# Kernel tuning notes

Hardware: AMD Instinct MI355X
Metric: run time of the kernel (lower is better)

The kernel has to match this reference:

```python
import jax, jax.numpy as jnp
import numpy as np

NEG_SLOPE = 0.01  # nn.LeakyReLU() default; module's alpha=-0.2 is unused
MASK_VAL = -1e12

N, IN_DIM, OUT_DIM = 4096, 512, 64


def setup_inputs() -> dict:
    key = jax.random.key(0)
    k1, k2, k3, k4 = jax.random.split(key, 4)
    input_h = jax.random.normal(k1, (N, IN_DIM), dtype=jnp.float32)
    adj = jax.random.randint(k2, (N, N), 0, 2, dtype=jnp.int32)
    W = jax.random.normal(k3, (IN_DIM, OUT_DIM), dtype=jnp.float32) * 0.05
    a = jax.random.normal(k4, (2 * OUT_DIM, 1), dtype=jnp.float32) * 0.05
    return {"input_h": input_h, "adj": adj, "W": W, "a": a}


def reference(input_h, adj, W, a):
    h = input_h @ W  # [N, D]
    D = h.shape[1]
    # e_ij = leakyrelu(a^T [h_i || h_j]) = leakyrelu(a1.h_i + a2.h_j)
    a1, a2 = a[:D, 0], a[D:, 0]
    s1 = h @ a1  # [N]
    s2 = h @ a2  # [N]
    e = s1[:, None] + s2[None, :]  # [N, N]
    e = jnp.where(e >= 0, e, NEG_SLOPE * e)  # LeakyReLU(0.01)
    scores = jnp.where(adj > 0, e, MASK_VAL)
    attention = jax.nn.softmax(scores, axis=1)
    # dropout omitted (eval mode / deterministic reference)
    return attention @ h  # [N, D]
```

## Files before the change

### kernel.cpp

```cpp
#include <hip/hip_runtime.h>
#include <hip/hip_bf16.h>

#define NN 4096
#define IN_DIM 512
#define OUT_D 64
#define LOG2E 1.44269504088896340736f

typedef __attribute__((ext_vector_type(8))) short short8v;
typedef __attribute__((ext_vector_type(4))) float f32x4;

__device__ __forceinline__ short to_bf16_rne(float x) {
  unsigned u = __builtin_bit_cast(unsigned, x);
  u = (u + 0x7FFFu + ((u >> 16) & 1u)) >> 16;
  return (short)u;
}
__device__ __forceinline__ float bf16_to_f(short h) {
  unsigned u = ((unsigned)(unsigned short)h) << 16;
  return __builtin_bit_cast(float, u);
}
__device__ __forceinline__ unsigned fkey(float f) {
  unsigned u = __builtin_bit_cast(unsigned, f);
  return u ^ ((unsigned)((int)u >> 31) | 0x80000000u);
}
__device__ __forceinline__ float funkey(unsigned k) {
  unsigned u = (k >> 31) ? (k ^ 0x80000000u) : ~k;
  return __builtin_bit_cast(float, u);
}

__global__ __launch_bounds__(256) void k_wpack(
    const float* __restrict__ W, short* __restrict__ Ahi, short* __restrict__ Alo,
    unsigned* __restrict__ s2key)
{
  int tid = blockIdx.x * 256 + threadIdx.x;
  if (tid == 0) *s2key = 0u;
  int l = tid & 63, t = (tid >> 6) & 15, m = tid >> 10;
  int dd = m * 16 + (l & 15);
  int kbase = t * 32 + 8 * (l >> 4);
  short8v hi, lo;
  #pragma unroll
  for (int r = 0; r < 8; ++r) {
    float w = W[(size_t)(kbase + r) * OUT_D + dd];
    short h = to_bf16_rne(w);
    hi[r] = h;
    lo[r] = to_bf16_rne(w - bf16_to_f(h));
  }
  *(short8v*)(Ahi + (size_t)tid * 8) = hi;
  *(short8v*)(Alo + (size_t)tid * 8) = lo;
}

__global__ __launch_bounds__(256) void k_h_mfma(
    const float* __restrict__ X,
    const short* __restrict__ Ahi, const short* __restrict__ Alo,
    const float* __restrict__ a,
    short* __restrict__ hbT, float* __restrict__ s1, float* __restrict__ s2,
    unsigned* __restrict__ s2key)
{
  __shared__ short xhi[16 * 512];
  __shared__ short xlo[16 * 512];
  __shared__ float sm1[4][16], sm2[4][16];
  int tid = threadIdx.x;
  int m = tid >> 6, l = tid & 63, lo = l & 15, g = l >> 4;
  int row0 = blockIdx.x * 16;

  #pragma unroll
  for (int i = 0; i < 4; ++i) {
    int flat = i * 2048 + tid * 8;
    int r = flat >> 9, k = flat & 511;
    float f[8];
    *(float4*)(f)     = *(const float4*)(X + (size_t)row0 * IN_DIM + flat);
    *(float4*)(f + 4) = *(const float4*)(X + (size_t)row0 * IN_DIM + flat + 4);
    short8v hi, lov;
    #pragma unroll
    for (int q = 0; q < 8; ++q) {
      short h = to_bf16_rne(f[q]);
      hi[q] = h;
      lov[q] = to_bf16_rne(f[q] - bf16_to_f(h));
    }
    int chunk = k >> 3;
    int dst = (r << 9) + ((chunk ^ (r & 7)) << 3);
    *(short8v*)(xhi + dst) = hi;
    *(short8v*)(xlo + dst) = lov;
  }
  __syncthreads();

  f32x4 acc = {0.f, 0.f, 0.f, 0.f};
  const short* ah = Ahi + ((size_t)(m * 16) * 64 + l) * 8;
  const short* al = Alo + ((size_t)(m * 16) * 64 + l) * 8;
  #pragma unroll
  for (int t = 0; t < 16; ++t) {
    int c = t * 4 + g;
    int src = (lo << 9) + ((c ^ (lo & 7)) << 3);
    short8v bhi = *(const short8v*)(xhi + src);
    short8v blo = *(const short8v*)(xlo + src);
    short8v fhi = *(const short8v*)(ah + (size_t)t * 64 * 8);
    short8v flo = *(const short8v*)(al + (size_t)t * 64 * 8);
    acc = __builtin_amdgcn_mfma_f32_16x16x32_bf16(fhi, bhi, acc, 0, 0, 0);
    acc = __builtin_amdgcn_mfma_f32_16x16x32_bf16(fhi, blo, acc, 0, 0, 0);
    acc = __builtin_amdgcn_mfma_f32_16x16x32_bf16(flo, bhi, acc, 0, 0, 0);
  }

  float p1 = 0.f, p2 = 0.f;
  #pragma unroll
  for (int q = 0; q < 4; ++q) {
    int d = m * 16 + 4 * g + q;
    hbT[(size_t)d * NN + row0 + lo] = to_bf16_rne(acc[q]);
    p1 = fmaf(acc[q], a[d], p1);
    p2 = fmaf(acc[q], a[OUT_D + d], p2);
  }
  p1 += __shfl_xor(p1, 16); p1 += __shfl_xor(p1, 32);
  p2 += __shfl_xor(p2, 16); p2 += __shfl_xor(p2, 32);
  if (l < 16) { sm1[m][l] = p1; sm2[m][l] = p2; }
  __syncthreads();
  if (tid < 16) {
    float v1 = (sm1[0][tid] + sm1[1][tid] + sm1[2][tid] + sm1[3][tid]) * LOG2E;
    float v2 = (sm2[0][tid] + sm2[1][tid] + sm2[2][tid] + sm2[3][tid]) * LOG2E;
    s1[row0 + tid] = v1;
    s2[row0 + tid] = v2;
    float v = v2;
    #pragma unroll
    for (int off = 8; off >= 1; off >>= 1) v = fmaxf(v, __shfl_xor(v, off));
    if (tid == 0) atomicMax(s2key, fkey(v));
  }
}

template<int JCHUNK>
__global__ __launch_bounds__(256) void k_attn(
    const int* __restrict__ adj, const short* __restrict__ hbT,
    const float* __restrict__ s1, const float* __restrict__ s2,
    const unsigned* __restrict__ s2keyp,
    float* __restrict__ accp, float* __restrict__ lpart)
{
  constexpr int NIT = JCHUNK / 32;
  int w  = threadIdx.x >> 6;
  int l  = threadIdx.x & 63;
  int lo = l & 15, g = l >> 4;
  int part  = blockIdx.y;
  int ibase = blockIdx.x * 64 + w * 16;
  int row   = ibase + lo;

  float s1v = s1[row];
  float x = s1v + funkey(*s2keyp);
  float M = fmaxf(x, 0.01f * x);

  f32x4 c0 = {0.f,0.f,0.f,0.f}, c1 = {0.f,0.f,0.f,0.f};
  f32x4 c2 = {0.f,0.f,0.f,0.f}, c3 = {0.f,0.f,0.f,0.f};
  float lsum = 0.f;

  const int* adjrow = adj + (size_t)row * NN;
  int jj = part * JCHUNK + g * 8;

  int4 pa0[2], pa1[2]; float4 ps0[2], ps1[2];
  #pragma unroll
  for (int p = 0; p < 2; ++p) {
    int j = jj + p * 32;
    pa0[p] = *(const int4*)(adjrow + j);
    pa1[p] = *(const int4*)(adjrow + j + 4);
    ps0[p] = *(const float4*)(s2 + j);
    ps1[p] = *(const float4*)(s2 + j + 4);
  }

  #pragma unroll
  for (int it = 0; it < NIT; ++it) {
    const int buf = it & 1;
    int4 a0 = pa0[buf], a1 = pa1[buf];
    float4 t0 = ps0[buf], t1 = ps1[buf];
    if (it + 2 < NIT) {
      int j = jj + (it + 2) * 32;
      pa0[buf] = *(const int4*)(adjrow + j);
      pa1[buf] = *(const int4*)(adjrow + j + 4);
      ps0[buf] = *(const float4*)(s2 + j);
      ps1[buf] = *(const float4*)(s2 + j + 4);
    }
    int jc = jj + it * 32;

    short8v b0 = *(const short8v*)(hbT + ((size_t)(lo)      << 12) + jc);
    short8v b1 = *(const short8v*)(hbT + ((size_t)(16 + lo) << 12) + jc);
    short8v b2 = *(const short8v*)(hbT + ((size_t)(32 + lo) << 12) + jc);
    short8v b3 = *(const short8v*)(hbT + ((size_t)(48 + lo) << 12) + jc);

    int av[8]; float sv[8];
    *(int4*)(av) = a0;  *(int4*)(av + 4) = a1;
    *(float4*)(sv) = t0; *(float4*)(sv + 4) = t1;

    short8v af;
    #pragma unroll
    for (int r = 0; r < 8; ++r) {
      float y = s1v + sv[r];
      float e = fmaxf(y, 0.01f * y);
      float p = exp2f(e - M);
      p = (av[r] > 0) ? p : 0.f;
      lsum += p;
      af[r] = to_bf16_rne(p);
    }

    c0 = __builtin_amdgcn_mfma_f32_16x16x32_bf16(af, b0, c0, 0, 0, 0);
    c1 = __builtin_amdgcn_mfma_f32_16x16x32_bf16(af, b1, c1, 0, 0, 0);
    c2 = __builtin_amdgcn_mfma_f32_16x16x32_bf16(af, b2, c2, 0, 0, 0);
    c3 = __builtin_amdgcn_mfma_f32_16x16x32_bf16(af, b3, c3, 0, 0, 0);
  }

  lsum += __shfl_xor(lsum, 16);
  lsum += __shfl_xor(lsum, 32);
  if (l < 16) lpart[(size_t)part * NN + ibase + l] = lsum;

  float* ap = accp + ((size_t)part * NN + ibase) * OUT_D;
  #pragma unroll
  for (int q = 0; q < 4; ++q) {
    int ri = g * 4 + q;
    ap[ri * OUT_D +  0 + lo] = c0[q];
    ap[ri * OUT_D + 16 + lo] = c1[q];
    ap[ri * OUT_D + 32 + lo] = c2[q];
    ap[ri * OUT_D + 48 + lo] = c3[q];
  }
}

__global__ __launch_bounds__(256) void k_attn_rt(
    const int* __restrict__ adj, const short* __restrict__ hbT,
    const float* __restrict__ s1, const float* __restrict__ s2,
    const unsigned* __restrict__ s2keyp,
    float* __restrict__ accp, float* __restrict__ lpart, int jchunk)
{
  int w  = threadIdx.x >> 6;
  int l  = threadIdx.x & 63;
  int lo = l & 15, g = l >> 4;
  int part  = blockIdx.y;
  int ibase = blockIdx.x * 64 + w * 16;
  int row   = ibase + lo;
  float s1v = s1[row];
  float x = s1v + funkey(*s2keyp);
  float M = fmaxf(x, 0.01f * x);
  f32x4 c0 = {0.f,0.f,0.f,0.f}, c1 = {0.f,0.f,0.f,0.f};
  f32x4 c2 = {0.f,0.f,0.f,0.f}, c3 = {0.f,0.f,0.f,0.f};
  float lsum = 0.f;
  const int* adjrow = adj + (size_t)row * NN;
  int jj = part * jchunk + g * 8;
  for (int js = 0; js < jchunk; js += 32, jj += 32) {
    int4 a0 = *(const int4*)(adjrow + jj);
    int4 a1 = *(const int4*)(adjrow + jj + 4);
    float4 t0 = *(const float4*)(s2 + jj);
    float4 t1 = *(const float4*)(s2 + jj + 4);
    short8v b0 = *(const short8v*)(hbT + ((size_t)(lo)      << 12) + jj);
    short8v b1 = *(const short8v*)(hbT + ((size_t)(16 + lo) << 12) + jj);
    short8v b2 = *(const short8v*)(hbT + ((size_t)(32 + lo) << 12) + jj);
    short8v b3 = *(const short8v*)(hbT + ((size_t)(48 + lo) << 12) + jj);
    int av[8]; float sv[8];
    *(int4*)(av) = a0;  *(int4*)(av + 4) = a1;
    *(float4*)(sv) = t0; *(float4*)(sv + 4) = t1;
    short8v af;
    #pragma unroll
    for (int r = 0; r < 8; ++r) {
      float y = s1v + sv[r];
      float e = fmaxf(y, 0.01f * y);
      float p = exp2f(e - M);
      p = (av[r] > 0) ? p : 0.f;
      lsum += p;
      af[r] = to_bf16_rne(p);
    }
    c0 = __builtin_amdgcn_mfma_f32_16x16x32_bf16(af, b0, c0, 0, 0, 0);
    c1 = __builtin_amdgcn_mfma_f32_16x16x32_bf16(af, b1, c1, 0, 0, 0);
    c2 = __builtin_amdgcn_mfma_f32_16x16x32_bf16(af, b2, c2, 0, 0, 0);
    c3 = __builtin_amdgcn_mfma_f32_16x16x32_bf16(af, b3, c3, 0, 0, 0);
  }
  lsum += __shfl_xor(lsum, 16);
  lsum += __shfl_xor(lsum, 32);
  if (l < 16) lpart[(size_t)part * NN + ibase + l] = lsum;
  float* ap = accp + ((size_t)part * NN + ibase) * OUT_D;
  #pragma unroll
  for (int q = 0; q < 4; ++q) {
    int ri = g * 4 + q;
    ap[ri * OUT_D +  0 + lo] = c0[q];
    ap[ri * OUT_D + 16 + lo] = c1[q];
    ap[ri * OUT_D + 32 + lo] = c2[q];
    ap[ri * OUT_D + 48 + lo] = c3[q];
  }
}

__global__ __launch_bounds__(256) void k_combine(
    const float* __restrict__ accp, const float* __restrict__ lpart,
    float* __restrict__ out, int npart)
{
  int idx = blockIdx.x * 256 + threadIdx.x;
  int i = idx >> 6;
  float s = 0.f, li = 0.f;
  for (int p = 0; p < npart; ++p) {
    s  += accp[(size_t)p * (NN * OUT_D) + idx];
    li += lpart[(size_t)p * NN + i];
  }
  out[idx] = s / li;
}

extern "C" void kernel_launch(void* const* d_in, const int* in_sizes, int n_in,
                              void* d_out, int out_size, void* d_ws, size_t ws_size,
                              hipStream_t stream)
{
  const float* X   = (const float*)d_in[0];
  const int*   adj = (const int*)d_in[1];
  const float* W   = (const float*)d_in[2];
  const float* a   = (const float*)d_in[3];
  float* out = (float*)d_out;

  char* ws = (char*)d_ws;
  size_t off = 0;
  float* s1  = (float*)(ws + off); off += NN * 4;
  float* s2  = (float*)(ws + off); off += NN * 4;
  unsigned* s2key = (unsigned*)(ws + off); off += 64;
  short* hbT = (short*)(ws + off); off += (size_t)OUT_D * NN * 2;
  short* Ahi = (short*)(ws + off); off += 4096 * 8 * 2;
  short* Alo = (short*)(ws + off); off += 4096 * 8 * 2;
  size_t fixed = off;

  size_t per_part = (size_t)(NN * OUT_D + NN) * 4;
  int npart = 1;
  for (int p = 16; p >= 1; p >>= 1)
    if (fixed + (size_t)p * per_part <= ws_size) { npart = p; break; }
  float* accp  = (float*)(ws + fixed);
  float* lpart = (float*)(ws + fixed + (size_t)npart * NN * OUT_D * 4);

  k_wpack<<<16, 256, 0, stream>>>(W, Ahi, Alo, s2key);
  k_h_mfma<<<NN / 16, 256, 0, stream>>>(X, Ahi, Alo, a, hbT, s1, s2, s2key);
  dim3 grid_attn(NN / 64, npart);
  if (npart == 16)
    k_attn<256><<<grid_attn, 256, 0, stream>>>(adj, hbT, s1, s2, s2key, accp, lpart);
  else if (npart == 8)
    k_attn<512><<<grid_attn, 256, 0, stream>>>(adj, hbT, s1, s2, s2key, accp, lpart);
  else
    k_attn_rt<<<grid_attn, 256, 0, stream>>>(adj, hbT, s1, s2, s2key, accp, lpart, NN / npart);
  k_combine<<<(NN * OUT_D) / 256, 256, 0, stream>>>(accp, lpart, out, npart);
}
```

Baseline: 54.08 us.

## Fuse split-K combine into attention kernel via last-block atomic counter

Each attention block increments a per-row-tile counter after writing its partial accumulators. The last block to finish for that tile sums the partial outputs and row sums across all parts and writes the normalized output. This removes the separate combine kernel launch and its extra pass over memory. In exchange it adds fences and atomics, and the final reduction runs serially in whichever block finishes last.

```diff
diff --git a/kernel.cpp b/kernel.cpp
--- a/kernel.cpp
+++ b/kernel.cpp
@@ -29,10 +29,13 @@
 
 __global__ __launch_bounds__(256) void k_wpack(
     const float* __restrict__ W, short* __restrict__ Ahi, short* __restrict__ Alo,
-    unsigned* __restrict__ s2key)
+    unsigned* __restrict__ s2key, int* __restrict__ cnt)
 {
   int tid = blockIdx.x * 256 + threadIdx.x;
-  if (tid == 0) *s2key = 0u;
+  if (blockIdx.x == 0) {
+    if (threadIdx.x == 0) *s2key = 0u;
+    if (threadIdx.x < NN / 64) cnt[threadIdx.x] = 0;
+  }
   int l = tid & 63, t = (tid >> 6) & 15, m = tid >> 10;
   int dd = m * 16 + (l & 15);
   int kbase = t * 32 + 8 * (l >> 4);
@@ -128,9 +131,12 @@
     const int* __restrict__ adj, const short* __restrict__ hbT,
     const float* __restrict__ s1, const float* __restrict__ s2,
     const unsigned* __restrict__ s2keyp,
-    float* __restrict__ accp, float* __restrict__ lpart)
+    float* __restrict__ accp, float* __restrict__ lpart,
+    int* __restrict__ cnt, float* __restrict__ out)
 {
   constexpr int NIT = JCHUNK / 32;
+  __shared__ int sflag;
+  __shared__ float srcp[64];
   int w  = threadIdx.x >> 6;
   int l  = threadIdx.x & 63;
   int lo = l & 15, g = l >> 4;
@@ -211,6 +217,34 @@
     ap[ri * OUT_D + 16 + lo] = c1[q];
     ap[ri * OUT_D + 32 + lo] = c2[q];
     ap[ri * OUT_D + 48 + lo] = c3[q];
+  }
+
+  __syncthreads();
+  if (threadIdx.x == 0) {
+    __threadfence();
+    int old = atomicAdd(&cnt[blockIdx.x], 1);
+    sflag = (old == (int)gridDim.y - 1);
+  }
+  __syncthreads();
+  if (!sflag) return;
+  __threadfence();
+
+  int npart = gridDim.y;
+  if (threadIdx.x < 64) {
+    float li = 0.f;
+    for (int p = 0; p < npart; ++p)
+      li += lpart[(size_t)p * NN + blockIdx.x * 64 + threadIdx.x];
+    srcp[threadIdx.x] = 1.0f / li;
+  }
+  __syncthreads();
+  int base = blockIdx.x * 64 * OUT_D;
+  #pragma unroll 4
+  for (int t = 0; t < 16; ++t) {
+    int idx = t * 256 + threadIdx.x;
+    float s = 0.f;
+    for (int p = 0; p < npart; ++p)
+      s += accp[(size_t)p * (NN * OUT_D) + base + idx];
+    out[base + idx] = s * srcp[idx >> 6];
   }
 }
 
@@ -304,6 +338,8 @@
   float* s1  = (float*)(ws + off); off += NN * 4;
   float* s2  = (float*)(ws + off); off += NN * 4;
   unsigned* s2key = (unsigned*)(ws + off); off += 64;
+  int* cnt   = (int*)(ws + off); off += (NN / 64) * 4;
+  off = (off + 63) & ~(size_t)63;
   short* hbT = (short*)(ws + off); off += (size_t)OUT_D * NN * 2;
   short* Ahi = (short*)(ws + off); off += 4096 * 8 * 2;
   short* Alo = (short*)(ws + off); off += 4096 * 8 * 2;
@@ -316,14 +352,15 @@
   float* accp  = (float*)(ws + fixed);
   float* lpart = (float*)(ws + fixed + (size_t)npart * NN * OUT_D * 4);
 
-  k_wpack<<<16, 256, 0, stream>>>(W, Ahi, Alo, s2key);
+  k_wpack<<<16, 256, 0, stream>>>(W, Ahi, Alo, s2key, cnt);
   k_h_mfma<<<NN / 16, 256, 0, stream>>>(X, Ahi, Alo, a, hbT, s1, s2, s2key);
   dim3 grid_attn(NN / 64, npart);
-  if (npart == 16)
-    k_attn<256><<<grid_attn, 256, 0, stream>>>(adj, hbT, s1, s2, s2key, accp, lpart);
-  else if (npart == 8)
-    k_attn<512><<<grid_attn, 256, 0, stream>>>(adj, hbT, s1, s2, s2key, accp, lpart);
-  else
+  if (npart == 16) {
+    k_attn<256><<<grid_attn, 256, 0, stream>>>(adj, hbT, s1, s2, s2key, accp, lpart, cnt, out);
+  } else if (npart == 8) {
+    k_attn<512><<<grid_attn, 256, 0, stream>>>(adj, hbT, s1, s2, s2key, accp, lpart, cnt, out);
+  } else {
     k_attn_rt<<<grid_attn, 256, 0, stream>>>(adj, hbT, s1, s2, s2key, accp, lpart, NN / npart);
-  k_combine<<<(NN * OUT_D) / 256, 256, 0, stream>>>(accp, lpart, out, npart);
-}
+    k_combine<<<(NN * OUT_D) / 256, 256, 0, stream>>>(accp, lpart, out, npart);
+  }
+}
```

Result: slower. 151.8 us (+180.7%).
